# Kernel tuning notes

Measured on AMD Instinct MI355X. Metric: run time of the kernel, lower is better.

## Reference

```python
import jax, jax.numpy as jnp
import numpy as np


def gcn_conv(x, src, dst, deg_inv_sqrt, W, b):
    # PyG GCNConv: h = x @ W, then symmetric-normalized scatter-add over edges
    # (edge list already includes self-loops; deg computed over it).
    h = x @ W                                   # [N, F_out]
    norm = deg_inv_sqrt[src] * deg_inv_sqrt[dst]  # [E]
    msgs = h[src] * norm[:, None]               # gather + scale
    out = jax.ops.segment_sum(msgs, dst, num_segments=x.shape[0])
    return out + b


def setup_inputs() -> dict:
    key = jax.random.key(0)
    k1, k2, k3, k4 = jax.random.split(key, 4)
    N, E, F_in, F_hid, F_out = 200000, 6400000, 128, 8, 16
    x = jax.random.normal(k1, (N, F_in), dtype=jnp.float32)
    edge_index = jax.random.randint(k2, (2, E), 0, N, dtype=jnp.int64)
    W1 = jax.random.normal(k3, (F_in, F_hid), dtype=jnp.float32) * (1.0 / np.sqrt(F_in))
    b1 = jnp.zeros((F_hid,), dtype=jnp.float32)
    W2 = jax.random.normal(k4, (F_hid, F_out), dtype=jnp.float32) * (1.0 / np.sqrt(F_hid))
    b2 = jnp.zeros((F_out,), dtype=jnp.float32)
    return {"x": x, "edge_index": edge_index, "W1": W1, "b1": b1, "W2": W2, "b2": b2}


def reference(x, edge_index, W1, b1, W2, b2):
    N = x.shape[0]
    # add self-loops (GCNConv default add_self_loops=True)
    loops = jnp.arange(N, dtype=edge_index.dtype)
    src = jnp.concatenate([edge_index[0], loops])
    dst = jnp.concatenate([edge_index[1], loops])
    deg = jax.ops.segment_sum(jnp.ones_like(dst, dtype=x.dtype), dst, num_segments=N)
    deg_inv_sqrt = jnp.where(deg > 0, jax.lax.rsqrt(deg), 0.0)
    h = jax.nn.relu(gcn_conv(x, src, dst, deg_inv_sqrt, W1, b1))
    # dropout is identity in eval mode (training=False)
    out = gcn_conv(h, src, dst, deg_inv_sqrt, W2, b2)
    return out
```

## Files before the change

### kernel.cpp

```cpp
#include <hip/hip_runtime.h>
#include <hip/hip_fp16.h>

#define F_IN  128
#define F_HID 8
#define F_OUT 16

#define SBSH  9
#define SBW   (1 << SBSH)
#define MAXB  400
#define BIN_CAP  32
#define FLUSH_G  16


typedef float f32x4 __attribute__((ext_vector_type(4)));

__global__ void init_gcur(int* __restrict__ gcur, int cap, int B) {
    int b = blockIdx.x * blockDim.x + threadIdx.x;
    if (b < B) gcur[b] = b * cap;
}

__global__ __launch_bounds__(512) void stage_bin(const int* __restrict__ ei,
                                                 int* __restrict__ gcur,
                                                 int* __restrict__ stage,
                                                 int E, int B, int per_block) {
    __shared__ int bin_cnt[MAXB];
    __shared__ int bin_buf[MAXB * BIN_CAP];
    for (int i = threadIdx.x; i < B; i += blockDim.x) bin_cnt[i] = 0;
    __syncthreads();
    const bool vec = ((E & 3) == 0);
    int base = blockIdx.x * per_block;
    int end  = min(E, base + per_block);
    for (int it = base; it < end; it += (int)blockDim.x * 4) {
        int e = it + (int)threadIdx.x * 4;
        int sv[4], dv[4], m4 = 0;
        if (vec && e + 3 < end) {
            int4 s4 = *(const int4*)(ei + e);
            int4 d4 = *(const int4*)(ei + E + e);
            sv[0] = s4.x; sv[1] = s4.y; sv[2] = s4.z; sv[3] = s4.w;
            dv[0] = d4.x; dv[1] = d4.y; dv[2] = d4.z; dv[3] = d4.w;
            m4 = 4;
        } else {
            for (int q = 0; e + q < end && q < 4; q++) { sv[q] = ei[e + q]; dv[q] = ei[E + e + q]; m4++; }
        }
        for (int q = 0; q < m4; q++) {
            int b   = dv[q] >> SBSH;
            int val = (sv[q] << SBSH) | (dv[q] & (SBW - 1));
            int pos = atomicAdd(&bin_cnt[b], 1);
            if (pos < BIN_CAP) {
                bin_buf[b * BIN_CAP + ((pos + b) & (BIN_CAP - 1))] = val;
            } else {
                int gp = atomicAdd(&gcur[b], 1);
                stage[gp] = val;
            }
        }
        __syncthreads();
        for (int b2 = threadIdx.x; b2 < B; b2 += blockDim.x) {
            int c = min(bin_cnt[b2], BIN_CAP);
            if (c >= FLUSH_G) {
                int m = c & ~(FLUSH_G - 1);
                int r = atomicAdd(&gcur[b2], m);
                for (int k = 0; k < m; k++)
                    stage[r + k] = bin_buf[b2 * BIN_CAP + ((k + b2) & (BIN_CAP - 1))];
                for (int k = m; k < c; k++)
                    bin_buf[b2 * BIN_CAP + ((k - m + b2) & (BIN_CAP - 1))] =
                        bin_buf[b2 * BIN_CAP + ((k + b2) & (BIN_CAP - 1))];
                bin_cnt[b2] = c - m;
            } else {
                bin_cnt[b2] = c;
            }
        }
        __syncthreads();
    }
    for (int b2 = threadIdx.x; b2 < B; b2 += blockDim.x) {
        int c = min(bin_cnt[b2], BIN_CAP);
        if (c > 0) {
            int r = atomicAdd(&gcur[b2], c);
            for (int k = 0; k < c; k++)
                stage[r + k] = bin_buf[b2 * BIN_CAP + ((k + b2) & (BIN_CAP - 1))];
        }
    }
}

__global__ __launch_bounds__(1024) void scatter_csr(const int* __restrict__ stage,
                                                    const int* __restrict__ gcur,
                                                    int cap,
                                                    int* __restrict__ cnt,
                                                    float* __restrict__ dis,
                                                    int* __restrict__ row_start,
                                                    int* __restrict__ csr, int n) {
    __shared__ int s0[SBW], s1[SBW];
    int b  = blockIdx.x;
    int nb = b << SBSH;
    int i  = threadIdx.x;
    if (i < SBW) s0[i] = 0;
    __syncthreads();
    int base = b * cap;
    int num  = gcur[b] - base;
    for (int k = i; k < num; k += 1024)
        atomicAdd(&s0[stage[base + k] & (SBW - 1)], 1);
    __syncthreads();
    int c = (i < SBW) ? s0[i] : 0;
    if (i < SBW && nb + i < n) { cnt[nb + i] = c; dis[nb + i] = rsqrtf((float)(c + 1)); }
    int* src = s0; int* dst = s1;
    for (int off = 1; off < SBW; off <<= 1) {
        if (i < SBW) dst[i] = src[i] + ((i >= off) ? src[i - off] : 0);
        __syncthreads();
        int* t = src; src = dst; dst = t;
    }
    if (i < SBW) {
        int e = base + src[i] - c;
        if (nb + i < n) row_start[nb + i] = e;
        dst[i] = e;
    }
    __syncthreads();
    for (int k = i; k < num; k += 1024) {
        int v = stage[base + k];
        int pos = atomicAdd(&dst[v & (SBW - 1)], 1);
        csr[pos] = v >> SBSH;
    }
}

__global__ __launch_bounds__(256) void gemm1(const float* __restrict__ x,
                                             const float* __restrict__ W1,
                                             const float* __restrict__ dis,
                                             __half* __restrict__ g1, int n) {
    __shared__ float w2[F_HID * F_IN];
    for (int i = threadIdx.x; i < F_HID * F_IN; i += blockDim.x) {
        int f = i >> 7, k = i & (F_IN - 1);
        w2[i] = W1[k * F_HID + f];
    }
    __syncthreads();
    int t = blockIdx.x * blockDim.x + threadIdx.x;
    int node = t >> 3, l = t & 7;
    if (node >= n) return;
    const f32x4* xr = (const f32x4*)(x + (size_t)node * F_IN);
    float acc[F_HID];
#pragma unroll
    for (int f = 0; f < F_HID; f++) acc[f] = 0.0f;
#pragma unroll
    for (int it = 0; it < 4; it++) {
        int j = l + it * 8;
        f32x4 v = __builtin_nontemporal_load(xr + j);
#pragma unroll
        for (int f = 0; f < F_HID; f++) {
            const float* wf = &w2[f * F_IN + j * 4];
            acc[f] += v[0] * wf[0] + v[1] * wf[1] + v[2] * wf[2] + v[3] * wf[3];
        }
    }
#pragma unroll
    for (int f = 0; f < F_HID; f++) {
        acc[f] += __shfl_xor(acc[f], 1);
        acc[f] += __shfl_xor(acc[f], 2);
        acc[f] += __shfl_xor(acc[f], 4);
    }
    if (l == 0) {
        float d = dis[node];
        __half2 h[4];
#pragma unroll
        for (int p = 0; p < 4; p++) h[p] = __floats2half2_rn(acc[2 * p] * d, acc[2 * p + 1] * d);
        *(uint4*)(g1 + (size_t)node * F_HID) = *(uint4*)h;
    }
}

__global__ __launch_bounds__(256) void aggregate_relu(const int* __restrict__ csr,
                                                      const int* __restrict__ row_start,
                                                      const int* __restrict__ cnt,
                                                      const float* __restrict__ dis,
                                                      const float* __restrict__ b1,
                                                      const __half* __restrict__ gin,
                                                      __half* __restrict__ gout, int n) {
    int t = blockIdx.x * blockDim.x + threadIdx.x;
    int node = t >> 2;
    int l = t & 3;
    if (node >= n) return;
    const __half2* g2 = (const __half2*)gin;
    int beg = row_start[node];
    int c   = cnt[node];
    float2 acc = __half22float2(g2[(unsigned)node * 4 + l]);
    int j = 0;
    int cm8 = c & ~7;
    for (; j < cm8; j += 8) {
        int va = __builtin_nontemporal_load(csr + beg + j + l);
        int vb = __builtin_nontemporal_load(csr + beg + j + 4 + l);
        int s0 = __shfl(va, 0, 4), s1 = __shfl(va, 1, 4);
        int s2 = __shfl(va, 2, 4), s3 = __shfl(va, 3, 4);
        int s4 = __shfl(vb, 0, 4), s5 = __shfl(vb, 1, 4);
        int s6 = __shfl(vb, 2, 4), s7 = __shfl(vb, 3, 4);
        __half2 h0 = g2[(unsigned)s0 * 4 + l];
        __half2 h1 = g2[(unsigned)s1 * 4 + l];
        __half2 h2 = g2[(unsigned)s2 * 4 + l];
        __half2 h3 = g2[(unsigned)s3 * 4 + l];
        __half2 h4 = g2[(unsigned)s4 * 4 + l];
        __half2 h5 = g2[(unsigned)s5 * 4 + l];
        __half2 h6 = g2[(unsigned)s6 * 4 + l];
        __half2 h7 = g2[(unsigned)s7 * 4 + l];
        float2 f0 = __half22float2(h0), f1 = __half22float2(h1);
        float2 f2 = __half22float2(h2), f3 = __half22float2(h3);
        float2 f4 = __half22float2(h4), f5 = __half22float2(h5);
        float2 f6 = __half22float2(h6), f7 = __half22float2(h7);
        acc.x += ((f0.x + f1.x) + (f2.x + f3.x)) + ((f4.x + f5.x) + (f6.x + f7.x));
        acc.y += ((f0.y + f1.y) + (f2.y + f3.y)) + ((f4.y + f5.y) + (f6.y + f7.y));
    }
    for (; j < c; j++) {
        int s = __builtin_nontemporal_load(csr + beg + j);
        float2 a = __half22float2(g2[(unsigned)s * 4 + l]);
        acc.x += a.x; acc.y += a.y;
    }
    float d = dis[node];
    float2 bv = *(const float2*)(b1 + 2 * l);
    float rx = fmaxf(fmaf(acc.x, d, bv.x), 0.0f) * d;
    float ry = fmaxf(fmaf(acc.y, d, bv.y), 0.0f) * d;
    ((__half2*)gout)[(unsigned)node * 4 + l] = __floats2half2_rn(rx, ry);
}

__global__ __launch_bounds__(256) void aggregate_out(const int* __restrict__ csr,
                                                     const int* __restrict__ row_start,
                                                     const int* __restrict__ cnt,
                                                     const float* __restrict__ dis,
                                                     const float* __restrict__ W2,
                                                     const float* __restrict__ b2,
                                                     const __half* __restrict__ gin,
                                                     float* __restrict__ out, int n) {
    int t = blockIdx.x * blockDim.x + threadIdx.x;
    int node = t >> 2;
    int l = t & 3;
    if (node >= n) return;
    const __half2* g2 = (const __half2*)gin;
    int beg = row_start[node];
    int c   = cnt[node];
    float2 acc = __half22float2(g2[(unsigned)node * 4 + l]);
    int j = 0;
    int cm8 = c & ~7;
    for (; j < cm8; j += 8) {
        int va = __builtin_nontemporal_load(csr + beg + j + l);
        int vb = __builtin_nontemporal_load(csr + beg + j + 4 + l);
        int s0 = __shfl(va, 0, 4), s1 = __shfl(va, 1, 4);
        int s2 = __shfl(va, 2, 4), s3 = __shfl(va, 3, 4);
        int s4 = __shfl(vb, 0, 4), s5 = __shfl(vb, 1, 4);
        int s6 = __shfl(vb, 2, 4), s7 = __shfl(vb, 3, 4);
        __half2 h0 = g2[(unsigned)s0 * 4 + l];
        __half2 h1 = g2[(unsigned)s1 * 4 + l];
        __half2 h2 = g2[(unsigned)s2 * 4 + l];
        __half2 h3 = g2[(unsigned)s3 * 4 + l];
        __half2 h4 = g2[(unsigned)s4 * 4 + l];
        __half2 h5 = g2[(unsigned)s5 * 4 + l];
        __half2 h6 = g2[(unsigned)s6 * 4 + l];
        __half2 h7 = g2[(unsigned)s7 * 4 + l];
        float2 f0 = __half22float2(h0), f1 = __half22float2(h1);
        float2 f2 = __half22float2(h2), f3 = __half22float2(h3);
        float2 f4 = __half22float2(h4), f5 = __half22float2(h5);
        float2 f6 = __half22float2(h6), f7 = __half22float2(h7);
        acc.x += ((f0.x + f1.x) + (f2.x + f3.x)) + ((f4.x + f5.x) + (f6.x + f7.x));
        acc.y += ((f0.y + f1.y) + (f2.y + f3.y)) + ((f4.y + f5.y) + (f6.y + f7.y));
    }
    for (; j < c; j++) {
        int s = __builtin_nontemporal_load(csr + beg + j);
        float2 a = __half22float2(g2[(unsigned)s * 4 + l]);
        acc.x += a.x; acc.y += a.y;
    }
    float d = dis[node];
    float ax = acc.x * d, ay = acc.y * d;
    float4 o = ((const float4*)b2)[l];
#pragma unroll
    for (int s = 0; s < 4; s++) {
        float axs = __shfl(ax, s, 4);
        float ays = __shfl(ay, s, 4);
        float4 w0 = ((const float4*)W2)[(2 * s) * 4 + l];
        float4 w1 = ((const float4*)W2)[(2 * s + 1) * 4 + l];
        o.x = fmaf(axs, w0.x, fmaf(ays, w1.x, o.x));
        o.y = fmaf(axs, w0.y, fmaf(ays, w1.y, o.y));
        o.z = fmaf(axs, w0.z, fmaf(ays, w1.z, o.z));
        o.w = fmaf(axs, w0.w, fmaf(ays, w1.w, o.w));
    }
    *(float4*)(out + (size_t)node * F_OUT + 4 * l) = o;
}

extern "C" void kernel_launch(void* const* d_in, const int* in_sizes, int n_in,
                              void* d_out, int out_size, void* d_ws, size_t ws_size,
                              hipStream_t stream) {
    const float* x  = (const float*)d_in[0];
    const int*   ei = (const int*)d_in[1];
    const float* W1 = (const float*)d_in[2];
    const float* b1 = (const float*)d_in[3];
    const float* W2 = (const float*)d_in[4];
    const float* b2 = (const float*)d_in[5];
    float* out = (float*)d_out;

    const int N = in_sizes[0] / F_IN;
    const int E = in_sizes[1] / 2;
    const int B = (N + SBW - 1) >> SBSH;

    int avg = (E + B - 1) / B;
    int cap = (avg + avg / 16 + 255) & ~255;

    int*    stage     = (int*)d_ws;
    int*    csr       = stage + (size_t)B * cap;
    float*  dis       = (float*)(csr + (size_t)B * cap);
    __half* gA        = (__half*)(dis + N);
    __half* gB        = (__half*)((int*)gA + (size_t)N * 4);
    int*    cnt       = (int*)gB + (size_t)N * 4;
    int*    row_start = cnt + N;
    int*    gcur      = row_start + N;

    const int BT = 256;
    dim3 thr(BT);
    dim3 blkG(((size_t)N * 8 + BT - 1) / BT);
    dim3 blkA(((size_t)N * 4 + BT - 1) / BT);

    int per_block = ((E + 639) / 640 + 2047) & ~2047;
    int SBLK = (E + per_block - 1) / per_block;

    init_gcur     <<<dim3((B + BT - 1) / BT), thr, 0, stream>>>(gcur, cap, B);
    stage_bin     <<<dim3(SBLK), dim3(512), 0, stream>>>(ei, gcur, stage, E, B, per_block);
    scatter_csr   <<<dim3(B),   dim3(1024), 0, stream>>>(stage, gcur, cap, cnt, dis, row_start, csr, N);
    gemm1         <<<blkG, thr, 0, stream>>>(x, W1, dis, gA, N);
    aggregate_relu<<<blkA, thr, 0, stream>>>(csr, row_start, cnt, dis, b1, gA, gB, N);
    aggregate_out <<<blkA, thr, 0, stream>>>(csr, row_start, cnt, dis, W2, b2, gB, out, N);
}
```

Measured before the change: 434.5 us.

## Prefetch edges and flush bins with wave-cooperative copies in stage_bin

New measurement: 924.5 us. 113% more time.

```diff
diff --git a/kernel.cpp b/kernel.cpp
--- a/kernel.cpp
+++ b/kernel.cpp
@@ -13,6 +13,7 @@
 
 
 typedef float f32x4 __attribute__((ext_vector_type(4)));
+typedef int   i32x4 __attribute__((ext_vector_type(4)));
 
 __global__ void init_gcur(int* __restrict__ gcur, int cap, int B) {
     int b = blockIdx.x * blockDim.x + threadIdx.x;
@@ -25,58 +26,85 @@
                                                  int E, int B, int per_block) {
     __shared__ int bin_cnt[MAXB];
     __shared__ int bin_buf[MAXB * BIN_CAP];
-    for (int i = threadIdx.x; i < B; i += blockDim.x) bin_cnt[i] = 0;
-    __syncthreads();
-    const bool vec = ((E & 3) == 0);
+    __shared__ int q[MAXB];
+    __shared__ int qn;
+    int tid  = threadIdx.x;
+    int wid  = tid >> 6;
+    int lane = tid & 63;
+    for (int i = tid; i < B; i += 512) bin_cnt[i] = 0;
     int base = blockIdx.x * per_block;
     int end  = min(E, base + per_block);
-    for (int it = base; it < end; it += (int)blockDim.x * 4) {
-        int e = it + (int)threadIdx.x * 4;
-        int sv[4], dv[4], m4 = 0;
-        if (vec && e + 3 < end) {
-            int4 s4 = *(const int4*)(ei + e);
-            int4 d4 = *(const int4*)(ei + E + e);
-            sv[0] = s4.x; sv[1] = s4.y; sv[2] = s4.z; sv[3] = s4.w;
-            dv[0] = d4.x; dv[1] = d4.y; dv[2] = d4.z; dv[3] = d4.w;
-            m4 = 4;
-        } else {
-            for (int q = 0; e + q < end && q < 4; q++) { sv[q] = ei[e + q]; dv[q] = ei[E + e + q]; m4++; }
-        }
-        for (int q = 0; q < m4; q++) {
-            int b   = dv[q] >> SBSH;
-            int val = (sv[q] << SBSH) | (dv[q] & (SBW - 1));
-            int pos = atomicAdd(&bin_cnt[b], 1);
-            if (pos < BIN_CAP) {
-                bin_buf[b * BIN_CAP + ((pos + b) & (BIN_CAP - 1))] = val;
-            } else {
-                int gp = atomicAdd(&gcur[b], 1);
-                stage[gp] = val;
+    int niter = per_block >> 12;
+    int e0 = base + tid * 8;
+    i32x4 sa, sb, da, db;
+    bool v = (e0 < end);
+    if (v) {
+        sa = *(const i32x4*)(ei + e0);     sb = *(const i32x4*)(ei + e0 + 4);
+        da = *(const i32x4*)(ei + E + e0); db = *(const i32x4*)(ei + E + e0 + 4);
+    }
+    __syncthreads();
+    for (int it = 0; it < niter; it++) {
+        if (tid == 0) qn = 0;
+        if (v) {
+            int sv[8] = {sa.x, sa.y, sa.z, sa.w, sb.x, sb.y, sb.z, sb.w};
+            int dv[8] = {da.x, da.y, da.z, da.w, db.x, db.y, db.z, db.w};
+#pragma unroll
+            for (int qq = 0; qq < 8; qq++) {
+                int b   = dv[qq] >> SBSH;
+                int val = (sv[qq] << SBSH) | (dv[qq] & (SBW - 1));
+                int pos = atomicAdd(&bin_cnt[b], 1);
+                if (pos < BIN_CAP) {
+                    bin_buf[b * BIN_CAP + ((pos + b) & (BIN_CAP - 1))] = val;
+                } else {
+                    int gp = atomicAdd(&gcur[b], 1);
+                    stage[gp] = val;
+                }
             }
         }
+        int en = e0 + 4096;
+        bool vn = (it + 1 < niter) && (en < end);
+        i32x4 nsa = {}, nsb = {}, nda = {}, ndb = {};
+        if (vn) {
+            nsa = __builtin_nontemporal_load((const i32x4*)(ei + en));
+            nsb = __builtin_nontemporal_load((const i32x4*)(ei + en + 4));
+            nda = __builtin_nontemporal_load((const i32x4*)(ei + E + en));
+            ndb = __builtin_nontemporal_load((const i32x4*)(ei + E + en + 4));
+        }
         __syncthreads();
-        for (int b2 = threadIdx.x; b2 < B; b2 += blockDim.x) {
-            int c = min(bin_cnt[b2], BIN_CAP);
-            if (c >= FLUSH_G) {
-                int m = c & ~(FLUSH_G - 1);
-                int r = atomicAdd(&gcur[b2], m);
-                for (int k = 0; k < m; k++)
-                    stage[r + k] = bin_buf[b2 * BIN_CAP + ((k + b2) & (BIN_CAP - 1))];
-                for (int k = m; k < c; k++)
-                    bin_buf[b2 * BIN_CAP + ((k - m + b2) & (BIN_CAP - 1))] =
-                        bin_buf[b2 * BIN_CAP + ((k + b2) & (BIN_CAP - 1))];
-                bin_cnt[b2] = c - m;
+        for (int b2 = tid; b2 < B; b2 += 512) {
+            int c = bin_cnt[b2]; if (c > BIN_CAP) c = BIN_CAP;
+            int m = c & ~(FLUSH_G - 1);
+            if (m) {
+                int s0 = c - m;
+                int idx = atomicAdd(&qn, 1);
+                q[idx] = b2 | (s0 << 9) | (m << 13);
+                bin_cnt[b2] = s0;
             } else {
                 bin_cnt[b2] = c;
             }
         }
         __syncthreads();
-    }
-    for (int b2 = threadIdx.x; b2 < B; b2 += blockDim.x) {
-        int c = min(bin_cnt[b2], BIN_CAP);
+        int nq = qn;
+        for (int w = wid; w < nq; w += 8) {
+            int qq = q[w];
+            int b2 = qq & 511, s0 = (qq >> 9) & 15, m = qq >> 13;
+            int r;
+            if (lane == 0) r = atomicAdd(&gcur[b2], m);
+            r = __shfl(r, 0);
+            if (lane < m)
+                stage[r + lane] = bin_buf[b2 * BIN_CAP + ((s0 + lane + b2) & (BIN_CAP - 1))];
+        }
+        __syncthreads();
+        sa = nsa; sb = nsb; da = nda; db = ndb; v = vn; e0 = en;
+    }
+    for (int w = wid; w < B; w += 8) {
+        int c = bin_cnt[w]; if (c > BIN_CAP) c = BIN_CAP;
         if (c > 0) {
-            int r = atomicAdd(&gcur[b2], c);
-            for (int k = 0; k < c; k++)
-                stage[r + k] = bin_buf[b2 * BIN_CAP + ((k + b2) & (BIN_CAP - 1))];
+            int r;
+            if (lane == 0) r = atomicAdd(&gcur[w], c);
+            r = __shfl(r, 0);
+            if (lane < c)
+                stage[r + lane] = bin_buf[w * BIN_CAP + ((lane + w) & (BIN_CAP - 1))];
         }
     }
 }
@@ -307,7 +335,8 @@
     dim3 blkG(((size_t)N * 8 + BT - 1) / BT);
     dim3 blkA(((size_t)N * 4 + BT - 1) / BT);
 
-    int per_block = ((E + 639) / 640 + 2047) & ~2047;
+    int per_block = ((E + 520) / 521 + 4095) & ~4095;
+    if (per_block < 4096) per_block = 4096;
     int SBLK = (E + per_block - 1) / per_block;
 
     init_gcur     <<<dim3((B + BT - 1) / BT), thr, 0, stream>>>(gcur, cap, B);
```
